# Kernel optimization log

Measured on AMD Instinct MI355X. Metric: run time of the kernel, lower is better.

Reference implementation:

```python
import jax, jax.numpy as jnp
import numpy as np

K1, K2, ALPHA = 0.01, 0.03, 0.84
SIGMA_LEVELS = (1, 2, 4, 7)

def _box_conv(x, k):
    # x: [B,1,H,W]; uniform k x k mean filter, padding k//2 (matches F.conv2d)
    p = k // 2
    w = jnp.ones((1, 1, k, k), x.dtype) / (k * k)
    return jax.lax.conv_general_dilated(
        x, w, window_strides=(1, 1), padding=((p, p), (p, p)),
        dimension_numbers=('NCHW', 'OIHW', 'NCHW'))

def _ssim_mean(X, Y, C1, C2, k):
    ux = _box_conv(X, k)
    uy = _box_conv(Y, k)
    uxx = _box_conv(X * X, k)
    uyy = _box_conv(Y * Y, k)
    uxy = _box_conv(X * Y, k)
    vx = uxx - ux * ux
    vy = uyy - uy * uy
    vxy = uxy - ux * uy
    A1 = 2 * ux * uy + C1
    A2 = 2 * vxy + C2
    B1 = ux * ux + uy * uy + C1
    B2 = vx + vy + C2
    S = (A1 * A2) / (B1 * B2)
    return jnp.mean(S)

def setup_inputs() -> dict:
    key = jax.random.key(0)
    k1, k2 = jax.random.split(key)
    B, H, W = 128, 384, 384
    X = jax.random.uniform(k1, (B, H, W), dtype=jnp.float32)
    Y = jax.random.uniform(k2, (B, H, W), dtype=jnp.float32)
    data_range = jnp.ones((B,), dtype=jnp.float32)
    return {"X": X, "Y": Y, "data_range": data_range}

def reference(X, Y, data_range):
    X4 = X[:, None, :, :]   # [B,1,H,W]
    Y4 = Y[:, None, :, :]
    dr = data_range[:, None, None, None]  # [B,1,1,1]
    C1 = (K1 * dr) ** 2
    C2 = (K2 * dr) ** 2
    # msssim = product of scalar SSIM means over sigma levels (ones_like * scalars).mean()
    msssim = jnp.float32(1.0)
    for k in SIGMA_LEVELS:
        msssim = msssim * _ssim_mean(X4, Y4, C1, C2, k)
    msssim_loss = 1.0 - msssim
    kM = SIGMA_LEVELS[-1]
    fX = _box_conv(X4, kM)
    fY = _box_conv(Y4, kM)
    l1 = jnp.mean(jnp.abs(fX - fY))
    return ALPHA * msssim_loss + (1.0 - ALPHA) * l1
```

## Files before the change

### kernel.cpp

```cpp
#include <hip/hip_runtime.h>


#define W 384
#define H 384
#define NB 128
#define NTILES 7
#define NPAIRS 4
#define NBLK (NTILES * NPAIRS * NB)

typedef __attribute__((ext_vector_type(2))) float f2;

__device__ __forceinline__ float bp(int addr, float v) {
    return __int_as_float(__builtin_amdgcn_ds_bpermute(addr, __float_as_int(v)));
}
__device__ __forceinline__ f2 f2s(float v) { f2 r; r.x = v; r.y = v; return r; }

__device__ __forceinline__ f2 ssim_pm2(f2 Vp, f2 Vm, f2 Vpp, f2 Vmm,
                                       float k2, float c1k42, float c2k42) {
    const f2 p2 = Vp * Vp;
    const f2 m2 = Vm * Vm;
    const f2 d  = p2 - m2;
    const f2 s  = p2 + m2;
    const f2 dq = Vpp - Vmm;
    const f2 sq = Vpp + Vmm;
    const f2 A1 = d + c1k42;
    const f2 B1 = s + c1k42;
    const f2 A2 = __builtin_elementwise_fma(f2s(k2), dq, -d) + c2k42;
    const f2 B2 = __builtin_elementwise_fma(f2s(k2), sq, -s) + c2k42;
    const f2 num = A1 * A2;
    const f2 den = B1 * B2;
    f2 r;
    r.x = num.x * __builtin_amdgcn_rcpf(den.x);
    r.y = num.y * __builtin_amdgcn_rcpf(den.y);
    return r;
}

__global__ __launch_bounds__(64, 2) void msssim_main(
    const float* __restrict__ X, const float* __restrict__ Y,
    const float* __restrict__ dr, float* __restrict__ part)
{
    const int lane = threadIdx.x;
    const int tile = blockIdx.x;
    const int g    = blockIdx.y;
    const int b    = blockIdx.z;

    const int c  = -3 + 56 * tile + lane;
    const int R0 = 48 * g;

    const float drb = dr[b];
    const float C1 = (0.01f * drb) * (0.01f * drb);
    const float C2 = (0.03f * drb) * (0.03f * drb);
    const float tC1 = 2.f * C1;
    const float C1_2 = C1 * 32.f,    C2_2 = C2 * 32.f;
    const float C1_4 = C1 * 512.f,   C2_4 = C2 * 512.f;
    const float C1_7 = C1 * 4802.f,  C2_7 = C2 * 4802.f;

    const float m1 = (lane >= 3 && lane <= 58 && c     <= 383) ? 1.f : 0.f;
    const float m2 = (lane >= 2 && lane <= 57 && c + 1 <= 384) ? 1.f : 0.f;
    const float m4 = (lane >= 1 && lane <= 56 && c + 2 <= 384) ? 1.f : 0.f;
    const float m7 = (             lane <= 55 && c + 3 <= 383) ? 1.f : 0.f;
    const f2 mk1 = f2s(m1);
    const f2 mk7 = f2s(m7);

    const int k2hi = (g == 3) ? 52 : 51;
    const int k4hi = (g == 3) ? 53 : 52;

    const float mcol = (c >= 0 && c < W) ? 1.f : 0.f;
    const int   cc   = c < 0 ? 0 : (c > W - 1 ? W - 1 : c);

    int ad[6];
#pragma unroll
    for (int d = 1; d <= 6; ++d) ad[d - 1] = ((lane + d) & 63) << 2;

    const float* __restrict__ Xb = X + (size_t)b * (H * W);
    const float* __restrict__ Yb = Y + (size_t)b * (H * W);

    f2 r2[4], r4[3][4], r7[6][4], v4s[4], v7s[4];
#pragma unroll
    for (int q = 0; q < 4; ++q) {
        r2[q] = f2s(0.f);
        r4[0][q] = r4[1][q] = r4[2][q] = f2s(0.f);
#pragma unroll
        for (int a = 0; a < 6; ++a) r7[a][q] = f2s(0.f);
        v4s[q] = f2s(0.f); v7s[q] = f2s(0.f);
    }

    f2 ss1v = f2s(0.f), ss2v = f2s(0.f), ss4v = f2s(0.f),
       ss7v = f2s(0.f), l1v  = f2s(0.f);

    const int u0 = R0 - 3;

    f2 rx[3], ry[3];
    auto loadv = [&](int u, int slot) {
        float x0 = 0.f, y0 = 0.f, x1 = 0.f, y1 = 0.f;
        if (u >= 0) {
            x0 = Xb[(size_t)u * W + cc];
            y0 = Yb[(size_t)u * W + cc];
        }
        const int r1 = u + 192;
        if (r1 < H) {
            x1 = Xb[(size_t)r1 * W + cc];
            y1 = Yb[(size_t)r1 * W + cc];
        }
        f2 vx; vx.x = x0; vx.y = x1;
        f2 vy; vy.x = y0; vy.y = y1;
        rx[slot] = vx; ry[slot] = vy;
    };

    f2 sp[3], sm[3], SRp[3][6], SRm[3][6];
    auto stageRow = [&](int slot, int buf) {
        const f2 p = (rx[slot] + ry[slot]) * f2s(mcol);
        const f2 m = (rx[slot] - ry[slot]) * f2s(mcol);
        sp[buf] = p; sm[buf] = m;
#pragma unroll
        for (int d = 0; d < 6; ++d) {
            f2 tp; tp.x = bp(ad[d], p.x); tp.y = bp(ad[d], p.y);
            f2 tm; tm.x = bp(ad[d], m.x); tm.y = bp(ad[d], m.y);
            SRp[buf][d] = tp; SRm[buf][d] = tm;
        }
    };

    loadv(u0,     0);
    loadv(u0 + 1, 1);
    loadv(u0 + 2, 2);
    stageRow(0, 0);
    stageRow(1, 1);

    for (int s = 0; s < 54; s += 6) {
#pragma unroll
        for (int ph = 0; ph < 6; ++ph) {
            const int t = s + ph;
            const int u = u0 + t;

            loadv(u + 3, ph % 3);

            const int cb = ph % 3;
            const f2 p0 = sp[cb], m0 = sm[cb];
            const f2 pp0 = p0 * p0, mm0 = m0 * m0;

            f2 W2[4], W4[4], W7[4];
            {
                const f2 e1 = SRp[cb][0], e2 = SRp[cb][1], e3 = SRp[cb][2];
                const f2 e4 = SRp[cb][3], e5 = SRp[cb][4], e6 = SRp[cb][5];
                const f2 f1 = SRm[cb][0], f2e = SRm[cb][1], f3 = SRm[cb][2];
                const f2 f4 = SRm[cb][3], f5 = SRm[cb][4], f6 = SRm[cb][5];
                W2[0] = p0 + e1;
                W4[0] = W2[0] + (e2 + e3);
                W7[0] = (W4[0] + (e4 + e5)) + e6;
                W2[1] = m0 + f1;
                W4[1] = W2[1] + (f2e + f3);
                W7[1] = (W4[1] + (f4 + f5)) + f6;
                const f2 s1 = e1 * e1, s2 = e2 * e2, s3 = e3 * e3;
                const f2 s4 = e4 * e4, s5 = e5 * e5, s6 = e6 * e6;
                W2[2] = pp0 + s1;
                W4[2] = W2[2] + (s2 + s3);
                W7[2] = (W4[2] + (s4 + s5)) + s6;
                const f2 t1 = f1 * f1, t2 = f2e * f2e, t3 = f3 * f3;
                const f2 t4 = f4 * f4, t5 = f5 * f5, t6 = f6 * f6;
                W2[3] = mm0 + t1;
                W4[3] = W2[3] + (t2 + t3);
                W7[3] = (W4[3] + (t4 + t5)) + t6;
            }

            f2 V2[4], V4[4], V7[4];
#pragma unroll
            for (int q = 0; q < 4; ++q) {
                V2[q] = W2[q] + r2[q];  r2[q] = W2[q];
                const f2 a4v = W4[q] + v4s[q];
                V4[q] = a4v;  v4s[q] = a4v - r4[2][q];
                r4[2][q] = r4[1][q]; r4[1][q] = r4[0][q]; r4[0][q] = W4[q];
                const f2 a7v = W7[q] + v7s[q];
                V7[q] = a7v;  v7s[q] = a7v - r7[5][q];
                r7[5][q] = r7[4][q]; r7[4][q] = r7[3][q]; r7[3][q] = r7[2][q];
                r7[2][q] = r7[1][q]; r7[1][q] = r7[0][q]; r7[0][q] = W7[q];
            }

            if (t >= 3 && t < 51) {
                const f2 num = (pp0 - mm0) + tC1;
                const f2 den = (pp0 + mm0) + tC1;
                f2 s1v;
                s1v.x = num.x * __builtin_amdgcn_rcpf(den.x);
                s1v.y = num.y * __builtin_amdgcn_rcpf(den.y);
                ss1v = __builtin_elementwise_fma(s1v, mk1, ss1v);
            }
            if (t >= 3 && t < k2hi) {
                f2 msk; msk.x = (t < 51) ? m2 : 0.f; msk.y = m2;
                ss2v = __builtin_elementwise_fma(
                    ssim_pm2(V2[0], V2[1], V2[2], V2[3], 4.f, C1_2, C2_2),
                    msk, ss2v);
            }
            if (t >= 4 && t < k4hi) {
                f2 msk; msk.x = (t < 52) ? m4 : 0.f; msk.y = m4;
                ss4v = __builtin_elementwise_fma(
                    ssim_pm2(V4[0], V4[1], V4[2], V4[3], 16.f, C1_4, C2_4),
                    msk, ss4v);
            }
            if (t >= 6) {
                ss7v = __builtin_elementwise_fma(
                    ssim_pm2(V7[0], V7[1], V7[2], V7[3], 49.f, C1_7, C2_7),
                    mk7, ss7v);
                f2 av; av.x = fabsf(V7[1].x); av.y = fabsf(V7[1].y);
                l1v = __builtin_elementwise_fma(av, mk7, l1v);
            }

            stageRow((ph + 2) % 3, (ph + 2) % 3);
        }
    }

    float ss1 = ss1v.x + ss1v.y;
    float ss2 = ss2v.x + ss2v.y;
    float ss4 = ss4v.x + ss4v.y;
    float ss7 = ss7v.x + ss7v.y;
    float l1  = l1v.x  + l1v.y;
#pragma unroll
    for (int d = 32; d > 0; d >>= 1) {
        ss1 += __shfl_down(ss1, d, 64);
        ss2 += __shfl_down(ss2, d, 64);
        ss4 += __shfl_down(ss4, d, 64);
        ss7 += __shfl_down(ss7, d, 64);
        l1  += __shfl_down(l1,  d, 64);
    }
    if (lane == 0) {
        const int bid = ((int)blockIdx.z * NPAIRS + (int)blockIdx.y) * NTILES
                        + (int)blockIdx.x;
        part[bid * 5 + 0] = ss1;
        part[bid * 5 + 1] = ss2;
        part[bid * 5 + 2] = ss4;
        part[bid * 5 + 3] = ss7;
        part[bid * 5 + 4] = l1;
    }
}

__global__ __launch_bounds__(256) void reduce_final(
    const float* __restrict__ part, float* __restrict__ out)
{
    const int lane = threadIdx.x & 63;
    const int wv   = threadIdx.x >> 6;
    double d[5] = {0, 0, 0, 0, 0};
    for (int i = threadIdx.x; i < NBLK; i += 256) {
#pragma unroll
        for (int q = 0; q < 5; ++q) d[q] += (double)part[i * 5 + q];
    }
#pragma unroll
    for (int s = 32; s > 0; s >>= 1) {
#pragma unroll
        for (int q = 0; q < 5; ++q) d[q] += __shfl_down(d[q], s, 64);
    }
    __shared__ double sd[4][5];
    if (lane == 0) {
#pragma unroll
        for (int q = 0; q < 5; ++q) sd[wv][q] = d[q];
    }
    __syncthreads();
    if (threadIdx.x == 0) {
        double a[5];
#pragma unroll
        for (int q = 0; q < 5; ++q)
            a[q] = sd[0][q] + sd[1][q] + sd[2][q] + sd[3][q];
        const double n384 = (double)NB * 384.0 * 384.0;
        const double n385 = (double)NB * 385.0 * 385.0;
        const double m  = (a[0] / n384) * (a[1] / n385) * (a[2] / n385) * (a[3] / n384);
        const double l1 = a[4] / 49.0 / n384;
        out[0] = (float)(0.84 * (1.0 - m) + 0.16 * l1);
    }
}

extern "C" void kernel_launch(void* const* d_in, const int* in_sizes, int n_in,
                              void* d_out, int out_size, void* d_ws, size_t ws_size,
                              hipStream_t stream) {
    const float* X  = (const float*)d_in[0];
    const float* Y  = (const float*)d_in[1];
    const float* dr = (const float*)d_in[2];
    float* out  = (float*)d_out;
    float* part = (float*)d_ws;

    dim3 grid(NTILES, NPAIRS, NB);
    msssim_main<<<grid, 64, 0, stream>>>(X, Y, dr, part);
    reduce_final<<<1, 256, 0, stream>>>(part, out);
}
```

Before: 212.5 us.

## Exchange neighbor columns via per-wave LDS float4 buffers instead of bpermute

Measured after the change: 201.2 us. 5.3% less time.

```diff
diff --git a/kernel.cpp b/kernel.cpp
--- a/kernel.cpp
+++ b/kernel.cpp
@@ -10,10 +10,8 @@
 
 typedef __attribute__((ext_vector_type(2))) float f2;
 
-__device__ __forceinline__ float bp(int addr, float v) {
-    return __int_as_float(__builtin_amdgcn_ds_bpermute(addr, __float_as_int(v)));
-}
 __device__ __forceinline__ f2 f2s(float v) { f2 r; r.x = v; r.y = v; return r; }
+__device__ __forceinline__ f2 mkf2(float a, float b) { f2 r; r.x = a; r.y = b; return r; }
 
 __device__ __forceinline__ f2 ssim_pm2(f2 Vp, f2 Vm, f2 Vpp, f2 Vmm,
                                        float k2, float c1k42, float c2k42) {
@@ -35,13 +33,14 @@
     return r;
 }
 
-__global__ __launch_bounds__(64, 2) void msssim_main(
+__global__ __launch_bounds__(256) void msssim_main(
     const float* __restrict__ X, const float* __restrict__ Y,
     const float* __restrict__ dr, float* __restrict__ part)
 {
-    const int lane = threadIdx.x;
+    const int lane = threadIdx.x & 63;
+    const int wv   = threadIdx.x >> 6;
     const int tile = blockIdx.x;
-    const int g    = blockIdx.y;
+    const int g    = wv;
     const int b    = blockIdx.z;
 
     const int c  = -3 + 56 * tile + lane;
@@ -68,9 +67,12 @@
     const float mcol = (c >= 0 && c < W) ? 1.f : 0.f;
     const int   cc   = c < 0 ? 0 : (c > W - 1 ? W - 1 : c);
 
-    int ad[6];
-#pragma unroll
-    for (int d = 1; d <= 6; ++d) ad[d - 1] = ((lane + d) & 63) << 2;
+    __shared__ float4 lds4[4][3][64];
+    float4* Lw = &lds4[wv][0][0];
+
+    int nidx[7];
+#pragma unroll
+    for (int d = 0; d < 7; ++d) nidx[d] = (lane + d) & 63;
 
     const float* __restrict__ Xb = X + (size_t)b * (H * W);
     const float* __restrict__ Yb = Y + (size_t)b * (H * W);
@@ -102,22 +104,21 @@
             x1 = Xb[(size_t)r1 * W + cc];
             y1 = Yb[(size_t)r1 * W + cc];
         }
-        f2 vx; vx.x = x0; vx.y = x1;
-        f2 vy; vy.x = y0; vy.y = y1;
-        rx[slot] = vx; ry[slot] = vy;
+        rx[slot] = mkf2(x0, x1);
+        ry[slot] = mkf2(y0, y1);
     };
 
-    f2 sp[3], sm[3], SRp[3][6], SRm[3][6];
     auto stageRow = [&](int slot, int buf) {
         const f2 p = (rx[slot] + ry[slot]) * f2s(mcol);
         const f2 m = (rx[slot] - ry[slot]) * f2s(mcol);
-        sp[buf] = p; sm[buf] = m;
-#pragma unroll
-        for (int d = 0; d < 6; ++d) {
-            f2 tp; tp.x = bp(ad[d], p.x); tp.y = bp(ad[d], p.y);
-            f2 tm; tm.x = bp(ad[d], m.x); tm.y = bp(ad[d], m.y);
-            SRp[buf][d] = tp; SRm[buf][d] = tm;
-        }
+        float4 v; v.x = p.x; v.y = p.y; v.z = m.x; v.w = m.y;
+        Lw[buf * 64 + lane] = v;
+    };
+
+    float4 R[7];
+    auto read7 = [&](int buf) {
+#pragma unroll
+        for (int d = 0; d < 7; ++d) R[d] = Lw[buf * 64 + nidx[d]];
     };
 
     loadv(u0,     0);
@@ -125,6 +126,7 @@
     loadv(u0 + 2, 2);
     stageRow(0, 0);
     stageRow(1, 1);
+    read7(0);
 
     for (int s = 0; s < 54; s += 6) {
 #pragma unroll
@@ -134,29 +136,30 @@
 
             loadv(u + 3, ph % 3);
 
-            const int cb = ph % 3;
-            const f2 p0 = sp[cb], m0 = sm[cb];
+            f2 ep[7], em[7];
+#pragma unroll
+            for (int d = 0; d < 7; ++d) {
+                ep[d] = mkf2(R[d].x, R[d].y);
+                em[d] = mkf2(R[d].z, R[d].w);
+            }
+            const f2 p0 = ep[0], m0 = em[0];
             const f2 pp0 = p0 * p0, mm0 = m0 * m0;
 
             f2 W2[4], W4[4], W7[4];
             {
-                const f2 e1 = SRp[cb][0], e2 = SRp[cb][1], e3 = SRp[cb][2];
-                const f2 e4 = SRp[cb][3], e5 = SRp[cb][4], e6 = SRp[cb][5];
-                const f2 f1 = SRm[cb][0], f2e = SRm[cb][1], f3 = SRm[cb][2];
-                const f2 f4 = SRm[cb][3], f5 = SRm[cb][4], f6 = SRm[cb][5];
-                W2[0] = p0 + e1;
-                W4[0] = W2[0] + (e2 + e3);
-                W7[0] = (W4[0] + (e4 + e5)) + e6;
-                W2[1] = m0 + f1;
-                W4[1] = W2[1] + (f2e + f3);
-                W7[1] = (W4[1] + (f4 + f5)) + f6;
-                const f2 s1 = e1 * e1, s2 = e2 * e2, s3 = e3 * e3;
-                const f2 s4 = e4 * e4, s5 = e5 * e5, s6 = e6 * e6;
+                W2[0] = p0 + ep[1];
+                W4[0] = W2[0] + (ep[2] + ep[3]);
+                W7[0] = (W4[0] + (ep[4] + ep[5])) + ep[6];
+                W2[1] = m0 + em[1];
+                W4[1] = W2[1] + (em[2] + em[3]);
+                W7[1] = (W4[1] + (em[4] + em[5])) + em[6];
+                const f2 s1 = ep[1] * ep[1], s2 = ep[2] * ep[2], s3 = ep[3] * ep[3];
+                const f2 s4 = ep[4] * ep[4], s5 = ep[5] * ep[5], s6 = ep[6] * ep[6];
                 W2[2] = pp0 + s1;
                 W4[2] = W2[2] + (s2 + s3);
                 W7[2] = (W4[2] + (s4 + s5)) + s6;
-                const f2 t1 = f1 * f1, t2 = f2e * f2e, t3 = f3 * f3;
-                const f2 t4 = f4 * f4, t5 = f5 * f5, t6 = f6 * f6;
+                const f2 t1 = em[1] * em[1], t2 = em[2] * em[2], t3 = em[3] * em[3];
+                const f2 t4 = em[4] * em[4], t5 = em[5] * em[5], t6 = em[6] * em[6];
                 W2[3] = mm0 + t1;
                 W4[3] = W2[3] + (t2 + t3);
                 W7[3] = (W4[3] + (t4 + t5)) + t6;
@@ -203,6 +206,8 @@
                 l1v = __builtin_elementwise_fma(av, mk7, l1v);
             }
 
+            read7((ph + 1) % 3);
+
             stageRow((ph + 2) % 3, (ph + 2) % 3);
         }
     }
@@ -221,8 +226,7 @@
         l1  += __shfl_down(l1,  d, 64);
     }
     if (lane == 0) {
-        const int bid = ((int)blockIdx.z * NPAIRS + (int)blockIdx.y) * NTILES
-                        + (int)blockIdx.x;
+        const int bid = ((int)blockIdx.z * NPAIRS + g) * NTILES + (int)blockIdx.x;
         part[bid * 5 + 0] = ss1;
         part[bid * 5 + 1] = ss2;
         part[bid * 5 + 2] = ss4;
@@ -274,7 +278,7 @@
     float* out  = (float*)d_out;
     float* part = (float*)d_ws;
 
-    dim3 grid(NTILES, NPAIRS, NB);
-    msssim_main<<<grid, 64, 0, stream>>>(X, Y, dr, part);
+    dim3 grid(NTILES, 1, NB);
+    msssim_main<<<grid, 256, 0, stream>>>(X, Y, dr, part);
     reduce_final<<<1, 256, 0, stream>>>(part, out);
 }
```
